# Kernel optimization log

Hardware: AMD Instinct MI355X
Metric: run time of the kernel (lower is better)

Reference implementation:

```python
import jax, jax.numpy as jnp
import numpy as np
from jax import lax


def _binarize(w):
    # XNOR-style sign binarization: sign(w) with sign(0) -> +1
    return jnp.where(w >= 0, 1.0, -1.0).astype(w.dtype)


def setup_inputs() -> dict:
    key = jax.random.key(0)
    kx, kw = jax.random.split(key)
    X = jax.random.normal(kx, (32, 256, 56, 56), dtype=jnp.float32)   # NCHW
    W = jax.random.normal(kw, (256, 256, 3, 3), dtype=jnp.float32)    # OIHW
    return {"X": X, "W": W}


def reference(X, W):
    Wb = _binarize(W)
    # F.conv2d default: padding=0 (VALID), stride=1
    out = lax.conv_general_dilated(
        X, Wb,
        window_strides=(1, 1),
        padding="VALID",
        dimension_numbers=("NCHW", "OIHW", "NCHW"),
    )
    return out  # [32, 256, 54, 54]
```

## Files before the change

kernel.cpp:

```cpp
#include <hip/hip_runtime.h>
#include <stdint.h>

typedef float f32x4 __attribute__((ext_vector_type(4)));
typedef __bf16 bf16x8 __attribute__((ext_vector_type(8)));
typedef unsigned short u16x8 __attribute__((ext_vector_type(8)));

#define NIMG 32
#define CIN  256
#define HWIN 3136
#define COUT 256
#define HWOUT 2916
#define NPOS 93312

#define XT_BYTES   ((size_t)NIMG*HWIN*CIN*2)
#define WT_OFF     (XT_BYTES + 8192)
#define WT_BYTES   ((size_t)36*256*64*2)
#define WS_NEED    (WT_OFF + WT_BYTES)

static __device__ __forceinline__ unsigned short f2bf(float f) {
    union { float f; uint32_t u; } v; v.f = f;
    return (unsigned short)((v.u + 0x7FFFu + ((v.u >> 16) & 1u)) >> 16);
}

static __device__ __forceinline__ void gload16(const void* g, void* l) {
    __builtin_amdgcn_global_load_lds(
        (const __attribute__((address_space(1))) void*)g,
        (__attribute__((address_space(3))) void*)l, 16, 0, 0);
}

static __device__ __forceinline__ uint32_t lds_a(const void* p) {
    return (uint32_t)(uintptr_t)(__attribute__((address_space(3))) const void*)p;
}

static __device__ __forceinline__ u16x8 ldsr(uint32_t addr) {
    u16x8 r;
    asm volatile("ds_read_b128 %0, %1" : "=v"(r) : "v"(addr));
    return r;
}

#define BAR()   __builtin_amdgcn_s_barrier()
#define SCB()   __builtin_amdgcn_sched_barrier(0)
#define LGKM0() do { asm volatile("s_waitcnt lgkmcnt(0)" ::: "memory"); SCB(); } while (0)
#define VM0()   asm volatile("s_waitcnt vmcnt(0)" ::: "memory")
#define PRIO1() __builtin_amdgcn_s_setprio(1)
#define PRIO0() __builtin_amdgcn_s_setprio(0)

#define MF(a_, b_, c_) __builtin_amdgcn_mfma_f32_16x16x32_bf16( \
    __builtin_bit_cast(bf16x8, a_), __builtin_bit_cast(bf16x8, b_), c_, 0, 0, 0)

#define CLUSTER(A0_, A1_, A2_, A3_, B0_, B1_, B2_, B3_) do {                       \
    acc[0][0]=MF(A0_,B0_,acc[0][0]); acc[1][0]=MF(A1_,B0_,acc[1][0]);              \
    acc[2][0]=MF(A2_,B0_,acc[2][0]); acc[3][0]=MF(A3_,B0_,acc[3][0]);              \
    acc[0][1]=MF(A0_,B1_,acc[0][1]); acc[1][1]=MF(A1_,B1_,acc[1][1]);              \
    acc[2][1]=MF(A2_,B1_,acc[2][1]); acc[3][1]=MF(A3_,B1_,acc[3][1]);              \
    acc[0][2]=MF(A0_,B2_,acc[0][2]); acc[1][2]=MF(A1_,B2_,acc[1][2]);              \
    acc[2][2]=MF(A2_,B2_,acc[2][2]); acc[3][2]=MF(A3_,B2_,acc[3][2]);              \
    acc[0][3]=MF(A0_,B3_,acc[0][3]); acc[1][3]=MF(A1_,B3_,acc[1][3]);              \
    acc[2][3]=MF(A2_,B3_,acc[2][3]); acc[3][3]=MF(A3_,B3_,acc[3][3]);              \
} while (0)

#define RD8(A0_, A1_, A2_, A3_, B0_, B1_, B2_, B3_, base_, ck_) do {               \
    A0_ = ldsr((base_) + ar0 + (ck_)); A1_ = ldsr((base_) + ar1 + (ck_));          \
    A2_ = ldsr((base_) + ar2 + (ck_)); A3_ = ldsr((base_) + ar3 + (ck_));          \
    B0_ = ldsr((base_) + br0 + (ck_)); B1_ = ldsr((base_) + br1 + (ck_));          \
    B2_ = ldsr((base_) + br2 + (ck_)); B3_ = ldsr((base_) + br3 + (ck_));          \
} while (0)

__global__ void wxform(const float* __restrict__ W, unsigned short* __restrict__ Wt) {
    int idx = blockIdx.x * 256 + threadIdx.x;
    int c6 = idx & 63;
    int o  = (idx >> 6) & 255;
    int cc = (idx >> 14) & 3;
    int k9 = idx >> 16;
    int c = cc * 64 + c6;
    float w = W[(size_t)(o * 256 + c) * 9 + k9];
    Wt[idx] = (w >= 0.0f) ? (unsigned short)0x3F80 : (unsigned short)0xBF80;
}

__global__ void xxform(const float* __restrict__ X, unsigned short* __restrict__ Xt) {
    __shared__ float tile[32][65];
    int bid = blockIdx.x;
    int hwc = bid % 49;
    int cc  = (bid / 49) & 7;
    int n   = bid / (49 * 8);
    int hw0 = hwc * 64;
    int c0  = cc * 32;
    int t = threadIdx.x;
    {
        int c = t >> 3;
        int w = (t & 7) * 8;
        const float* src = X + (size_t)(n * CIN + c0 + c) * HWIN + hw0 + w;
        float4 a = *(const float4*)src;
        float4 b = *(const float4*)(src + 4);
        tile[c][w + 0] = a.x; tile[c][w + 1] = a.y; tile[c][w + 2] = a.z; tile[c][w + 3] = a.w;
        tile[c][w + 4] = b.x; tile[c][w + 5] = b.y; tile[c][w + 6] = b.z; tile[c][w + 7] = b.w;
    }
    __syncthreads();
    {
        int w  = t >> 2;
        int cb = (t & 3) * 8;
        u16x8 v;
        #pragma unroll
        for (int j = 0; j < 8; ++j) v[j] = f2bf(tile[cb + j][w]);
        *(u16x8*)(Xt + (size_t)(n * HWIN + hw0 + w) * 256 + c0 + cb) = v;
    }
}

__global__ __launch_bounds__(256, 2)
void bconv_gemm(const unsigned short* __restrict__ Xt,
                const unsigned short* __restrict__ Wt,
                float* __restrict__ out) {
    __shared__ __align__(16) char smem[65536];

    const int t    = threadIdx.x;
    const int wid  = t >> 6;
    const int lane = t & 63;
    const int l15  = lane & 15;
    const int lg   = lane >> 4;
    const int wr   = wid >> 1;
    const int wc   = wid & 1;
    const int ob   = blockIdx.x;
    const uint32_t P0 = blockIdx.y * 128u;

    const uint32_t colxB = (uint32_t)(((t & 7) ^ ((t >> 3) & 7)) << 4);
    const uint32_t rowt  = (uint32_t)(t >> 3);

    const char* pA0 = (const char*)Wt + (size_t)ob * 16384 + rowt * 128 + colxB;

    const char* bB[4];
    #pragma unroll
    for (int r = 0; r < 4; ++r) {
        uint32_t pos = P0 + (uint32_t)(r * 32) + rowt;
        uint32_t ni = pos / (uint32_t)HWOUT;
        uint32_t rm = pos - ni * HWOUT;
        uint32_t ph = rm / 54u;
        uint32_t pw = rm - ph * 54u;
        bB[r] = (const char*)Xt + (size_t)(ni * HWIN + ph * 56u + pw) * 512 + colxB;
    }

    const uint32_t x7  = (uint32_t)(l15 & 7);
    const uint32_t ck0 = ((((uint32_t)lg) ^ x7) << 4);
    const uint32_t ck1 = (((4u | (uint32_t)lg) ^ x7) << 4);
    const uint32_t ar0 = (uint32_t)(wr * 64 + 0 * 16 + l15) * 128u;
    const uint32_t ar1 = (uint32_t)(wr * 64 + 1 * 16 + l15) * 128u;
    const uint32_t ar2 = (uint32_t)(wr * 64 + 2 * 16 + l15) * 128u;
    const uint32_t ar3 = (uint32_t)(wr * 64 + 3 * 16 + l15) * 128u;
    const uint32_t br0 = 16384u + (uint32_t)(wc * 64 + 0 * 16 + l15) * 128u;
    const uint32_t br1 = 16384u + (uint32_t)(wc * 64 + 1 * 16 + l15) * 128u;
    const uint32_t br2 = 16384u + (uint32_t)(wc * 64 + 2 * 16 + l15) * 128u;
    const uint32_t br3 = 16384u + (uint32_t)(wc * 64 + 3 * 16 + l15) * 128u;

    const uint32_t E = lds_a(smem);
    const uint32_t O = E + 32768u;

    f32x4 acc[4][4];
    #pragma unroll
    for (int m = 0; m < 4; ++m)
        #pragma unroll
        for (int n = 0; n < 4; ++n)
            acc[m][n] = (f32x4){0.f, 0.f, 0.f, 0.f};

    auto STAGE = [&](uint32_t off, int kt, uint32_t kof) {
        const char* p = pA0 + (uint32_t)kt * 32768u;
        #pragma unroll
        for (int r = 0; r < 4; ++r)
            gload16(p + r * 4096, smem + off + r * 4096 + (size_t)t * 16);
        #pragma unroll
        for (int r = 0; r < 4; ++r)
            gload16(bB[r] + kof, smem + off + 16384 + r * 4096 + (size_t)t * 16);
    };

    uint32_t cc2 = 2, k32 = 0, koff2 = 256;

    STAGE(0u, 0, 0u);
    STAGE(32768u, 1, 128u);
    VM0();
    BAR();
    SCB();

    u16x8 s0a0, s0a1, s0a2, s0a3, s0b0, s0b1, s0b2, s0b3;
    u16x8 s1a0, s1a1, s1a2, s1a3, s1b0, s1b1, s1b2, s1b3;

    RD8(s0a0, s0a1, s0a2, s0a3, s0b0, s0b1, s0b2, s0b3, E, ck0);
    LGKM0();

    for (int kt = 0; kt < 36; ++kt) {
        const uint32_t cur = (kt & 1) ? O : E;
        const uint32_t nxt = (kt & 1) ? E : O;

        RD8(s1a0, s1a1, s1a2, s1a3, s1b0, s1b1, s1b2, s1b3, cur, ck1);
        SCB();
        PRIO1();
        CLUSTER(s0a0, s0a1, s0a2, s0a3, s0b0, s0b1, s0b2, s0b3);
        PRIO0();
        LGKM0();
        VM0();
        BAR();
        SCB();
        if (kt < 34) {
            STAGE(cur, kt + 2, koff2);
            if (cc2 == 3) { cc2 = 0; koff2 += ((k32 == 2) ? 54u : 1u) * 512u - 384u; k32 = (k32 == 2) ? 0u : k32 + 1u; }
            else          { cc2++; koff2 += 128u; }
        }
        if (kt < 35) {
            RD8(s0a0, s0a1, s0a2, s0a3, s0b0, s0b1, s0b2, s0b3, nxt, ck0);
            SCB();
            PRIO1();
            CLUSTER(s1a0, s1a1, s1a2, s1a3, s1b0, s1b1, s1b2, s1b3);
            PRIO0();
            LGKM0();
        } else {
            PRIO1();
            CLUSTER(s1a0, s1a1, s1a2, s1a3, s1b0, s1b1, s1b2, s1b3);
            PRIO0();
        }
    }

    const int orow0 = ob * 128 + wr * 64;
    #pragma unroll
    for (int n = 0; n < 4; ++n) {
        uint32_t P = P0 + (uint32_t)(wc * 64 + n * 16 + l15);
        uint32_t ni = P / (uint32_t)HWOUT;
        uint32_t rm = P - ni * HWOUT;
        float* ob_ = out + (size_t)(ni * 256u + orow0) * HWOUT + rm;
        #pragma unroll
        for (int m = 0; m < 4; ++m)
            #pragma unroll
            for (int r = 0; r < 4; ++r)
                ob_[(size_t)(m * 16 + lg * 4 + r) * HWOUT] = acc[m][n][r];
    }
}

__global__ void bconv_fallback(const float* __restrict__ X, const float* __restrict__ W,
                               float* __restrict__ out) {
    size_t idx = (size_t)blockIdx.x * 256 + threadIdx.x;
    int ow = (int)(idx % 54);
    int oh = (int)((idx / 54) % 54);
    int o  = (int)((idx / 2916) % 256);
    int n  = (int)(idx / 746496);
    float s = 0.f;
    for (int c = 0; c < 256; ++c) {
        const float* xr = X + ((size_t)(n * 256 + c) * 56 + oh) * 56 + ow;
        const float* wr = W + (size_t)(o * 256 + c) * 9;
        #pragma unroll
        for (int kh = 0; kh < 3; ++kh)
            #pragma unroll
            for (int kw = 0; kw < 3; ++kw) {
                float w = wr[kh * 3 + kw];
                float x = xr[kh * 56 + kw];
                s += (w >= 0.f) ? x : -x;
            }
    }
    out[idx] = s;
}

extern "C" void kernel_launch(void* const* d_in, const int* in_sizes, int n_in,
                              void* d_out, int out_size, void* d_ws, size_t ws_size,
                              hipStream_t stream) {
    const float* X = (const float*)d_in[0];
    const float* W = (const float*)d_in[1];
    float* out = (float*)d_out;

    if (ws_size < WS_NEED) {
        bconv_fallback<<<93312, 256, 0, stream>>>(X, W, out);
        return;
    }
    unsigned short* Xt = (unsigned short*)d_ws;
    unsigned short* Wt = (unsigned short*)((char*)d_ws + WT_OFF);

    wxform<<<2304, 256, 0, stream>>>(W, Wt);
    xxform<<<12544, 256, 0, stream>>>(X, Xt);

    dim3 grid(2, 729);
    bconv_gemm<<<grid, 256, 0, stream>>>(Xt, Wt, out);
}
```

Measured before the change: 148.2 us.

## Load weight tiles straight to registers, halve LDS, swizzle blocks across XCDs

The A (weight) operand no longer goes through LDS. Each wave loads its weight fragments from global memory straight into registers, one k-step ahead, and waits with partial vmcnt counts. Only the B (activation) tile is staged in LDS, which halves shared memory to 32KB and removes the A-side LDS reads. The grid becomes 1D with an XCD-aware block remap, so blocks sharing activation tiles land on the same XCD for L2 reuse. The cost is more VGPRs for double-buffered A fragments and uncoalesced per-lane global loads, which may hurt occupancy or latency hiding.

```diff
diff --git a/kernel.cpp b/kernel.cpp
--- a/kernel.cpp
+++ b/kernel.cpp
@@ -41,6 +41,8 @@
 #define BAR()   __builtin_amdgcn_s_barrier()
 #define SCB()   __builtin_amdgcn_sched_barrier(0)
 #define LGKM0() do { asm volatile("s_waitcnt lgkmcnt(0)" ::: "memory"); SCB(); } while (0)
+#define VM12()  asm volatile("s_waitcnt vmcnt(12)" ::: "memory")
+#define VM8()   asm volatile("s_waitcnt vmcnt(8)" ::: "memory")
 #define VM0()   asm volatile("s_waitcnt vmcnt(0)" ::: "memory")
 #define PRIO1() __builtin_amdgcn_s_setprio(1)
 #define PRIO0() __builtin_amdgcn_s_setprio(0)
@@ -59,11 +61,41 @@
     acc[2][3]=MF(A2_,B3_,acc[2][3]); acc[3][3]=MF(A3_,B3_,acc[3][3]);              \
 } while (0)
 
-#define RD8(A0_, A1_, A2_, A3_, B0_, B1_, B2_, B3_, base_, ck_) do {               \
-    A0_ = ldsr((base_) + ar0 + (ck_)); A1_ = ldsr((base_) + ar1 + (ck_));          \
-    A2_ = ldsr((base_) + ar2 + (ck_)); A3_ = ldsr((base_) + ar3 + (ck_));          \
-    B0_ = ldsr((base_) + br0 + (ck_)); B1_ = ldsr((base_) + br1 + (ck_));          \
-    B2_ = ldsr((base_) + br2 + (ck_)); B3_ = ldsr((base_) + br3 + (ck_));          \
+#define LOADA(AN, kt_) do {                                          \
+    const char* _p0 = pA_lo + (size_t)(uint32_t)(kt_) * 32768u;      \
+    const char* _p1 = pA_hi + (size_t)(uint32_t)(kt_) * 32768u;      \
+    AN##0 = *(const u16x8*)(_p0);                                    \
+    AN##1 = *(const u16x8*)(_p0 + 64);                               \
+    AN##2 = *(const u16x8*)(_p0 + 2048);                             \
+    AN##3 = *(const u16x8*)(_p0 + 2048 + 64);                        \
+    AN##4 = *(const u16x8*)(_p1);                                    \
+    AN##5 = *(const u16x8*)(_p1 + 64);                               \
+    AN##6 = *(const u16x8*)(_p1 + 2048);                             \
+    AN##7 = *(const u16x8*)(_p1 + 2048 + 64);                        \
+} while (0)
+
+#define GITER(kt_, CUR, NXT, CUROFF, AC, AN, F_LA, F_ST, F_CONT) do {       \
+    V0 = ldsr((CUR) + br0 + ck1); V1 = ldsr((CUR) + br1 + ck1);             \
+    V2 = ldsr((CUR) + br2 + ck1); V3 = ldsr((CUR) + br3 + ck1);             \
+    if (F_LA) { LOADA(AN, (kt_) + 1); VM12(); } else { VM0(); }             \
+    SCB();                                                                   \
+    PRIO1(); CLUSTER(AC##0, AC##2, AC##4, AC##6, U0, U1, U2, U3); PRIO0();  \
+    LGKM0();                                                                 \
+    if (F_CONT) {                                                            \
+        VM8(); BAR(); SCB();                                                 \
+        if (F_ST) {                                                          \
+            STAGEB(CUROFF, koff2);                                           \
+            if (cc2 == 3) { cc2 = 0;                                         \
+                koff2 += ((k32 == 2) ? 54u : 1u) * 512u - 384u;              \
+                k32 = (k32 == 2) ? 0u : k32 + 1u; }                          \
+            else { cc2++; koff2 += 128u; }                                   \
+        }                                                                    \
+        U0 = ldsr((NXT) + br0 + ck0); U1 = ldsr((NXT) + br1 + ck0);         \
+        U2 = ldsr((NXT) + br2 + ck0); U3 = ldsr((NXT) + br3 + ck0);         \
+        SCB();                                                               \
+    }                                                                        \
+    PRIO1(); CLUSTER(AC##1, AC##3, AC##5, AC##7, V0, V1, V2, V3); PRIO0();  \
+    if (F_CONT) { LGKM0(); }                                                 \
 } while (0)
 
 __global__ void wxform(const float* __restrict__ W, unsigned short* __restrict__ Wt) {
@@ -110,7 +142,7 @@
 void bconv_gemm(const unsigned short* __restrict__ Xt,
                 const unsigned short* __restrict__ Wt,
                 float* __restrict__ out) {
-    __shared__ __align__(16) char smem[65536];
+    __shared__ __align__(16) char smem[32768];
 
     const int t    = threadIdx.x;
     const int wid  = t >> 6;
@@ -119,13 +151,19 @@
     const int lg   = lane >> 4;
     const int wr   = wid >> 1;
     const int wc   = wid & 1;
-    const int ob   = blockIdx.x;
-    const uint32_t P0 = blockIdx.y * 128u;
+
+    const uint32_t bid = blockIdx.x;
+    const uint32_t xcd = bid & 7u;
+    const uint32_t j8  = bid >> 3;
+    const uint32_t swz = (xcd < 2u ? xcd * 183u : 366u + (xcd - 2u) * 182u) + j8;
+    const int      ob  = (int)(swz & 1u);
+    const uint32_t P0  = (swz >> 1) * 128u;
 
     const uint32_t colxB = (uint32_t)(((t & 7) ^ ((t >> 3) & 7)) << 4);
     const uint32_t rowt  = (uint32_t)(t >> 3);
 
-    const char* pA0 = (const char*)Wt + (size_t)ob * 16384 + rowt * 128 + colxB;
+    const char* pA_lo = (const char*)Wt + (size_t)(ob * 128 + wr * 64 + l15) * 128 + lg * 16;
+    const char* pA_hi = pA_lo + 4096;
 
     const char* bB[4];
     #pragma unroll
@@ -141,17 +179,13 @@
     const uint32_t x7  = (uint32_t)(l15 & 7);
     const uint32_t ck0 = ((((uint32_t)lg) ^ x7) << 4);
     const uint32_t ck1 = (((4u | (uint32_t)lg) ^ x7) << 4);
-    const uint32_t ar0 = (uint32_t)(wr * 64 + 0 * 16 + l15) * 128u;
-    const uint32_t ar1 = (uint32_t)(wr * 64 + 1 * 16 + l15) * 128u;
-    const uint32_t ar2 = (uint32_t)(wr * 64 + 2 * 16 + l15) * 128u;
-    const uint32_t ar3 = (uint32_t)(wr * 64 + 3 * 16 + l15) * 128u;
-    const uint32_t br0 = 16384u + (uint32_t)(wc * 64 + 0 * 16 + l15) * 128u;
-    const uint32_t br1 = 16384u + (uint32_t)(wc * 64 + 1 * 16 + l15) * 128u;
-    const uint32_t br2 = 16384u + (uint32_t)(wc * 64 + 2 * 16 + l15) * 128u;
-    const uint32_t br3 = 16384u + (uint32_t)(wc * 64 + 3 * 16 + l15) * 128u;
+    const uint32_t br0 = (uint32_t)(wc * 64 + 0 * 16 + l15) * 128u;
+    const uint32_t br1 = (uint32_t)(wc * 64 + 1 * 16 + l15) * 128u;
+    const uint32_t br2 = (uint32_t)(wc * 64 + 2 * 16 + l15) * 128u;
+    const uint32_t br3 = (uint32_t)(wc * 64 + 3 * 16 + l15) * 128u;
 
     const uint32_t E = lds_a(smem);
-    const uint32_t O = E + 32768u;
+    const uint32_t O = E + 16384u;
 
     f32x4 acc[4][4];
     #pragma unroll
@@ -160,61 +194,34 @@
         for (int n = 0; n < 4; ++n)
             acc[m][n] = (f32x4){0.f, 0.f, 0.f, 0.f};
 
-    auto STAGE = [&](uint32_t off, int kt, uint32_t kof) {
-        const char* p = pA0 + (uint32_t)kt * 32768u;
+    auto STAGEB = [&](uint32_t bufoff, uint32_t kof) {
         #pragma unroll
         for (int r = 0; r < 4; ++r)
-            gload16(p + r * 4096, smem + off + r * 4096 + (size_t)t * 16);
-        #pragma unroll
-        for (int r = 0; r < 4; ++r)
-            gload16(bB[r] + kof, smem + off + 16384 + r * 4096 + (size_t)t * 16);
+            gload16(bB[r] + kof, smem + bufoff + r * 4096 + (size_t)t * 16);
     };
 
     uint32_t cc2 = 2, k32 = 0, koff2 = 256;
 
-    STAGE(0u, 0, 0u);
-    STAGE(32768u, 1, 128u);
+    u16x8 AE0, AE1, AE2, AE3, AE4, AE5, AE6, AE7;
+    u16x8 AO0, AO1, AO2, AO3, AO4, AO5, AO6, AO7;
+    u16x8 U0, U1, U2, U3, V0, V1, V2, V3;
+
+    STAGEB(0u, 0u);
+    STAGEB(16384u, 128u);
+    LOADA(AE, 0);
     VM0();
     BAR();
     SCB();
-
-    u16x8 s0a0, s0a1, s0a2, s0a3, s0b0, s0b1, s0b2, s0b3;
-    u16x8 s1a0, s1a1, s1a2, s1a3, s1b0, s1b1, s1b2, s1b3;
-
-    RD8(s0a0, s0a1, s0a2, s0a3, s0b0, s0b1, s0b2, s0b3, E, ck0);
+    U0 = ldsr(E + br0 + ck0); U1 = ldsr(E + br1 + ck0);
+    U2 = ldsr(E + br2 + ck0); U3 = ldsr(E + br3 + ck0);
     LGKM0();
 
-    for (int kt = 0; kt < 36; ++kt) {
-        const uint32_t cur = (kt & 1) ? O : E;
-        const uint32_t nxt = (kt & 1) ? E : O;
-
-        RD8(s1a0, s1a1, s1a2, s1a3, s1b0, s1b1, s1b2, s1b3, cur, ck1);
-        SCB();
-        PRIO1();
-        CLUSTER(s0a0, s0a1, s0a2, s0a3, s0b0, s0b1, s0b2, s0b3);
-        PRIO0();
-        LGKM0();
-        VM0();
-        BAR();
-        SCB();
-        if (kt < 34) {
-            STAGE(cur, kt + 2, koff2);
-            if (cc2 == 3) { cc2 = 0; koff2 += ((k32 == 2) ? 54u : 1u) * 512u - 384u; k32 = (k32 == 2) ? 0u : k32 + 1u; }
-            else          { cc2++; koff2 += 128u; }
-        }
-        if (kt < 35) {
-            RD8(s0a0, s0a1, s0a2, s0a3, s0b0, s0b1, s0b2, s0b3, nxt, ck0);
-            SCB();
-            PRIO1();
-            CLUSTER(s1a0, s1a1, s1a2, s1a3, s1b0, s1b1, s1b2, s1b3);
-            PRIO0();
-            LGKM0();
-        } else {
-            PRIO1();
-            CLUSTER(s1a0, s1a1, s1a2, s1a3, s1b0, s1b1, s1b2, s1b3);
-            PRIO0();
-        }
-    }
+    for (int g = 0; g < 17; ++g) {
+        GITER(2 * g,     E, O, 0u,      AE, AO, 1, 1, 1);
+        GITER(2 * g + 1, O, E, 16384u,  AO, AE, 1, 1, 1);
+    }
+    GITER(34, E, O, 0u,     AE, AO, 1, 0, 1);
+    GITER(35, O, E, 16384u, AO, AE, 0, 0, 0);
 
     const int orow0 = ob * 128 + wr * 64;
     #pragma unroll
@@ -271,6 +278,5 @@
     wxform<<<2304, 256, 0, stream>>>(W, Wt);
     xxform<<<12544, 256, 0, stream>>>(X, Xt);
 
-    dim3 grid(2, 729);
-    bconv_gemm<<<grid, 256, 0, stream>>>(Xt, Wt, out);
-}
+    bconv_gemm<<<1458, 256, 0, stream>>>(Xt, Wt, out);
+}
```

New measurement: 262.0 us. +76.8%, slower.
